# Optimization experiments

Measured on AMD Instinct MI355X. Metric: run time of the kernel, lower is better.

Reference implementation:

```python
import jax, jax.numpy as jnp
import numpy as np

B, S, D = 8, 1024, 1024  # module requires S == D for the k + w_bias broadcast
MAX_LEN = 1024


def setup_inputs() -> dict:
    key = jax.random.key(0)
    ks = jax.random.split(key, 10)
    scale = 0.02
    return {
        "x": jax.random.normal(ks[0], (B, S, D), dtype=jnp.float32),
        "wq_w": scale * jax.random.normal(ks[1], (D, D), dtype=jnp.float32),
        "wq_b": jnp.zeros((D,), dtype=jnp.float32),
        "wk_w": scale * jax.random.normal(ks[2], (D, D), dtype=jnp.float32),
        "wk_b": jnp.zeros((D,), dtype=jnp.float32),
        "wv_w": scale * jax.random.normal(ks[3], (D, D), dtype=jnp.float32),
        "wv_b": jnp.zeros((D,), dtype=jnp.float32),
        "w": 0.01 * jax.random.normal(ks[4], (MAX_LEN, MAX_LEN), dtype=jnp.float32),
        "out_w": scale * jax.random.normal(ks[5], (D, D), dtype=jnp.float32),
        "out_b": jnp.zeros((D,), dtype=jnp.float32),
    }


def reference(x, wq_w, wq_b, wk_w, wk_b, wv_w, wv_b, w, out_w, out_b):
    # torch nn.Linear: y = x @ W.T + b
    q = x @ wq_w.T + wq_b            # [B,S,D]
    k = x @ wk_w.T + wk_b            # [B,S,D]
    v = x @ wv_w.T + wv_b            # [B,S,D]
    seq_len = x.shape[1]
    w_bias = w[:seq_len, :seq_len][None]          # [1,S,S]
    # NB: original code broadcasts [B,S,D] + [1,S,S]; requires D == S.
    num = jnp.matmul(jnp.exp(k + w_bias), v)      # [B,S,D]
    den = jnp.matmul(jnp.exp(w_bias), jnp.exp(k)) # [B,S,D]
    y = jax.nn.sigmoid(q) * num / den
    return y @ out_w.T + out_b
```

## Files before the change

kernel.cpp:

```cpp
#include <hip/hip_runtime.h>
#include <hip/hip_bf16.h>


typedef float  f32x4  __attribute__((ext_vector_type(4)));
typedef short  short8 __attribute__((ext_vector_type(8)));
typedef __bf16 bf16x8 __attribute__((ext_vector_type(8)));

__device__ __forceinline__ ushort f2bf(float f){
  uint u = __builtin_bit_cast(uint, f);
  u += 0x7fffu + ((u >> 16) & 1u);
  return (ushort)(u >> 16);
}
__device__ __forceinline__ float bf2f(ushort u){
  uint v = ((uint)u) << 16;
  return __builtin_bit_cast(float, v);
}

__device__ __forceinline__ void gload16(const ushort* g, ushort* l){
  __builtin_amdgcn_global_load_lds(
      (const __attribute__((address_space(1))) void*)g,
      (__attribute__((address_space(3))) void*)l, 16, 0, 0);
}

__device__ __forceinline__ f32x4 mfma16(short8 a, short8 b, f32x4 c){
  return __builtin_amdgcn_mfma_f32_16x16x32_bf16(
      __builtin_bit_cast(bf16x8, a), __builtin_bit_cast(bf16x8, b), c, 0, 0, 0);
}

template<int EPI>
__global__ __launch_bounds__(256) void gemm_bt(
    const ushort* __restrict__ A, const ushort* __restrict__ B,
    void* __restrict__ C, const float* __restrict__ bias,
    int N, int K, long sA, long sB, long sC)
{
  __shared__ ushort As[128 * 64] __attribute__((aligned(16)));
  __shared__ ushort Bs[128 * 64] __attribute__((aligned(16)));

  const int tid  = threadIdx.x;
  const int lane = tid & 63;
  const int wid  = tid >> 6;
  const int wm   = wid >> 1;
  const int wn   = wid & 1;
  const long z   = blockIdx.z;
  const long tileM = (long)blockIdx.y * 128;
  const long tileN = (long)blockIdx.x * 128;

  const ushort* Ab = A + z * sA + tileM * K;
  const ushort* Bb = B + z * sB + tileN * K;

  long gOff[4]; int lOff[4];
#pragma unroll
  for (int j = 0; j < 4; ++j) {
    int chunk = j * 256 + tid;
    int row   = chunk >> 3;
    int c16   = (chunk & 7) ^ (row & 7);
    gOff[j]   = (long)row * K + c16 * 8;
    lOff[j]   = chunk * 8;
  }

  f32x4 acc[4][4];
#pragma unroll
  for (int i = 0; i < 4; ++i)
#pragma unroll
    for (int j = 0; j < 4; ++j) acc[i][j] = (f32x4)0.f;

  const int rA0 = wm * 64 + (lane & 15);
  const int rB0 = wn * 64 + (lane & 15);
  const int cw0 = lane >> 4;

  for (int kt = 0; kt < K; kt += 64) {
    __syncthreads();
#pragma unroll
    for (int j = 0; j < 4; ++j) {
      gload16(Ab + gOff[j] + kt, &As[lOff[j]]);
      gload16(Bb + gOff[j] + kt, &Bs[lOff[j]]);
    }
    __syncthreads();

    short8 af[4][2], bf[4][2];
#pragma unroll
    for (int f = 0; f < 4; ++f) {
      int ra = rA0 + f * 16;
      int rb = rB0 + f * 16;
#pragma unroll
      for (int kk = 0; kk < 2; ++kk) {
        af[f][kk] = *(const short8*)&As[ra * 64 + (((kk * 4 + cw0) ^ (ra & 7)) * 8)];
        bf[f][kk] = *(const short8*)&Bs[rb * 64 + (((kk * 4 + cw0) ^ (rb & 7)) * 8)];
      }
    }
#pragma unroll
    for (int kk = 0; kk < 2; ++kk)
#pragma unroll
      for (int fi = 0; fi < 4; ++fi)
#pragma unroll
        for (int fj = 0; fj < 4; ++fj)
          acc[fi][fj] = mfma16(af[fi][kk], bf[fj][kk], acc[fi][fj]);
  }

#pragma unroll
  for (int fi = 0; fi < 4; ++fi) {
    long gm0 = tileM + wm * 64 + fi * 16 + (lane >> 4) * 4;
#pragma unroll
    for (int fj = 0; fj < 4; ++fj) {
      long gn = tileN + wn * 64 + fj * 16 + (lane & 15);
      float bv = bias ? bias[gn] : 0.f;
      if (EPI == 0) {
        ushort* Cp = (ushort*)C + z * sC;
#pragma unroll
        for (int r = 0; r < 4; ++r)
          Cp[(gm0 + r) * (long)N + gn] = f2bf(acc[fi][fj][r] + bv);
      } else {
        float* Cp = (float*)C + z * sC;
#pragma unroll
        for (int r = 0; r < 4; ++r)
          Cp[(gm0 + r) * (long)N + gn] = acc[fi][fj][r] + bv;
      }
    }
  }
}

__global__ void cvt_x(const float* __restrict__ in, ushort* __restrict__ out){
  long i4 = ((long)blockIdx.x * 256 + threadIdx.x) * 4;
  float4 v = *(const float4*)&in[i4];
  ushort4 o;
  o.x = f2bf(v.x); o.y = f2bf(v.y); o.z = f2bf(v.z); o.w = f2bf(v.w);
  *(ushort4*)&out[i4] = o;
}

__global__ void prep(const float* __restrict__ wq, const float* __restrict__ wk,
                     const float* __restrict__ wv, const float* __restrict__ ow,
                     const float* __restrict__ w,
                     const float* __restrict__ bq, const float* __restrict__ bk,
                     const float* __restrict__ bv,
                     ushort* __restrict__ wcat, ushort* __restrict__ owb,
                     ushort* __restrict__ ewb, float* __restrict__ bcat)
{
  long i4 = ((long)blockIdx.x * 256 + threadIdx.x) * 4;
  const long MB = 1048576;
  if (i4 < 3 * MB) {
    const float* src = (i4 < MB) ? wq : (i4 < 2 * MB ? wk : wv);
    long off = i4 & (MB - 1);
    float4 v = *(const float4*)&src[off];
    ushort4 o; o.x=f2bf(v.x); o.y=f2bf(v.y); o.z=f2bf(v.z); o.w=f2bf(v.w);
    *(ushort4*)&wcat[i4] = o;
  } else if (i4 < 4 * MB) {
    long off = i4 - 3 * MB;
    float4 v = *(const float4*)&ow[off];
    ushort4 o; o.x=f2bf(v.x); o.y=f2bf(v.y); o.z=f2bf(v.z); o.w=f2bf(v.w);
    *(ushort4*)&owb[off] = o;
  } else if (i4 < 5 * MB) {
    long off = i4 - 4 * MB;
    float4 v = *(const float4*)&w[off];
    ushort4 o;
    o.x=f2bf(expf(v.x)); o.y=f2bf(expf(v.y)); o.z=f2bf(expf(v.z)); o.w=f2bf(expf(v.w));
    *(ushort4*)&ewb[off] = o;
  } else {
    long i = i4 - 5 * MB;
    if (i < 3072) {
      const float* src = (i < 1024) ? bq : (i < 2048 ? bk : bv);
      long off = i & 1023;
      *(float4*)&bcat[i] = *(const float4*)&src[off];
    }
  }
}

__global__ void ew_E(const ushort* __restrict__ qkv, const float* __restrict__ w,
                     ushort* __restrict__ E)
{
  long e4 = ((long)blockIdx.x * 256 + threadIdx.x) * 4;
  long m = e4 >> 10;
  int  j = (int)(e4 & 1023);
  int  s = (int)(m & 1023);
  ushort4 kv = *(const ushort4*)&qkv[m * 3072 + 1024 + j];
  float4  wv = *(const float4*)&w[(long)s * 1024 + j];
  ushort4 o;
  o.x = f2bf(expf(bf2f(kv.x) + wv.x));
  o.y = f2bf(expf(bf2f(kv.y) + wv.y));
  o.z = f2bf(expf(bf2f(kv.z) + wv.z));
  o.w = f2bf(expf(bf2f(kv.w) + wv.w));
  *(ushort4*)&E[e4] = o;
}

template<bool DOEXP>
__global__ void transpose_seg(const ushort* __restrict__ qkv,
                              ushort* __restrict__ dst, int colOff)
{
  __shared__ float tile[32][33];
  int b  = blockIdx.z;
  int s0 = blockIdx.y * 32, d0 = blockIdx.x * 32;
  int tx = threadIdx.x, ty = threadIdx.y;
#pragma unroll
  for (int i = 0; i < 4; ++i) {
    int s = s0 + ty + i * 8;
    float f = bf2f(qkv[((long)(b * 1024 + s)) * 3072 + colOff + d0 + tx]);
    if (DOEXP) f = expf(f);
    tile[ty + i * 8][tx] = f;
  }
  __syncthreads();
#pragma unroll
  for (int i = 0; i < 4; ++i) {
    int d = d0 + ty + i * 8;
    dst[((long)b * 1024 + d) * 1024 + s0 + tx] = f2bf(tile[tx][ty + i * 8]);
  }
}

__global__ void ew_y(const ushort* __restrict__ qkv, const ushort* __restrict__ num,
                     const ushort* __restrict__ den, ushort* __restrict__ y)
{
  long e4 = ((long)blockIdx.x * 256 + threadIdx.x) * 4;
  long m = e4 >> 10;
  int  d = (int)(e4 & 1023);
  ushort4 q4 = *(const ushort4*)&qkv[m * 3072 + d];
  ushort4 n4 = *(const ushort4*)&num[e4];
  ushort4 d4 = *(const ushort4*)&den[e4];
  ushort4 o;
  {
    float q = bf2f(q4.x), s = 1.f / (1.f + expf(-q));
    o.x = f2bf(s * bf2f(n4.x) / bf2f(d4.x));
  }
  {
    float q = bf2f(q4.y), s = 1.f / (1.f + expf(-q));
    o.y = f2bf(s * bf2f(n4.y) / bf2f(d4.y));
  }
  {
    float q = bf2f(q4.z), s = 1.f / (1.f + expf(-q));
    o.z = f2bf(s * bf2f(n4.z) / bf2f(d4.z));
  }
  {
    float q = bf2f(q4.w), s = 1.f / (1.f + expf(-q));
    o.w = f2bf(s * bf2f(n4.w) / bf2f(d4.w));
  }
  *(ushort4*)&y[e4] = o;
}

extern "C" void kernel_launch(void* const* d_in, const int* in_sizes, int n_in,
                              void* d_out, int out_size, void* d_ws, size_t ws_size,
                              hipStream_t stream)
{
  const float* x     = (const float*)d_in[0];
  const float* wq_w  = (const float*)d_in[1];
  const float* wq_b  = (const float*)d_in[2];
  const float* wk_w  = (const float*)d_in[3];
  const float* wk_b  = (const float*)d_in[4];
  const float* wv_w  = (const float*)d_in[5];
  const float* wv_b  = (const float*)d_in[6];
  const float* w     = (const float*)d_in[7];
  const float* out_w = (const float*)d_in[8];
  const float* out_b = (const float*)d_in[9];
  float* out = (float*)d_out;

  const long MB = 1048576;
  char* ws = (char*)d_ws;
  size_t o = 0;
  auto alloc = [&](size_t bytes){ size_t r = o; o += (bytes + 255) & ~(size_t)255; return r; };

  ushort* xb   = (ushort*)(ws + alloc(8192 * 1024 * 2));
  ushort* wcat = (ushort*)(ws + alloc(3072 * 1024 * 2));
  ushort* owb  = (ushort*)(ws + alloc(1024 * 1024 * 2));
  ushort* ewb  = (ushort*)(ws + alloc(1024 * 1024 * 2));
  float*  bcat = (float*) (ws + alloc(3072 * 4));
  ushort* qkvb = (ushort*)(ws + alloc(8192 * 3072 * 2));
  ushort* Eb   = (ushort*)(ws + alloc(8 * MB * 2));
  ushort* vTb  = (ushort*)(ws + alloc(8 * MB * 2));
  ushort* EKTb = (ushort*)(ws + alloc(8 * MB * 2));
  ushort* numb = (ushort*)(ws + alloc(8 * MB * 2));
  ushort* denb = (ushort*)(ws + alloc(8 * MB * 2));
  ushort* yb   = (ushort*)(ws + alloc(8 * MB * 2));
  (void)ws_size; (void)in_sizes; (void)n_in; (void)out_size;

  cvt_x<<<8192, 256, 0, stream>>>(x, xb);
  prep<<<5123, 256, 0, stream>>>(wq_w, wk_w, wv_w, out_w, w,
                                 wq_b, wk_b, wv_b, wcat, owb, ewb, bcat);

  gemm_bt<0><<<dim3(24, 64, 1), 256, 0, stream>>>(
      xb, wcat, qkvb, bcat, 3072, 1024, 0, 0, 0);

  ew_E<<<8192, 256, 0, stream>>>(qkvb, w, Eb);
  transpose_seg<false><<<dim3(32, 32, 8), dim3(32, 8), 0, stream>>>(qkvb, vTb, 2048);
  transpose_seg<true ><<<dim3(32, 32, 8), dim3(32, 8), 0, stream>>>(qkvb, EKTb, 1024);

  gemm_bt<0><<<dim3(8, 8, 8), 256, 0, stream>>>(
      Eb, vTb, numb, nullptr, 1024, 1024, MB, MB, MB);
  gemm_bt<0><<<dim3(8, 8, 8), 256, 0, stream>>>(
      ewb, EKTb, denb, nullptr, 1024, 1024, 0, MB, MB);

  ew_y<<<8192, 256, 0, stream>>>(qkvb, numb, denb, yb);

  gemm_bt<1><<<dim3(8, 64, 1), 256, 0, stream>>>(
      yb, owb, out, out_b, 1024, 1024, 0, 0, 0);
}
```

Before: 296.9 us.

## Add 256x256 tiled bf16 GEMM and merge num/den batched GEMMs into one launch

Introduces a 512-thread GEMM kernel with 256x256 output tiles, a 4-stage LDS ring filled by direct global-to-LDS loads, swizzled LDS layout, and split MFMA phases with priority hints. It is used for the QKV projection and for a single launch that covers both the numerator and denominator batched GEMMs through a z-split. The goal is more data reuse per tile and less launch overhead, at the cost of fewer blocks (tail and occupancy risk) and heavy register pressure from 128 accumulators per lane.

```diff
diff --git a/kernel.cpp b/kernel.cpp
--- a/kernel.cpp
+++ b/kernel.cpp
@@ -25,6 +25,126 @@
 __device__ __forceinline__ f32x4 mfma16(short8 a, short8 b, f32x4 c){
   return __builtin_amdgcn_mfma_f32_16x16x32_bf16(
       __builtin_bit_cast(bf16x8, a), __builtin_bit_cast(bf16x8, b), c, 0, 0, 0);
+}
+
+__global__ __launch_bounds__(512, 2) void gemm256(
+    const ushort* __restrict__ A0, long sA0,
+    const ushort* __restrict__ B0, long sB0,
+    ushort* __restrict__ C0, long sC0,
+    const ushort* __restrict__ A1, long sA1,
+    const ushort* __restrict__ B1, long sB1,
+    ushort* __restrict__ C1, long sC1,
+    const float* __restrict__ bias, int N, int zsplit)
+{
+  __shared__ ushort sh[65536] __attribute__((aligned(16)));
+
+  const int tid  = threadIdx.x;
+  const int lane = tid & 63;
+  const int wid  = tid >> 6;
+  const int wm   = wid >> 2;
+  const int wn   = wid & 3;
+  const long tileM = (long)blockIdx.y * 256;
+  const long tileN = (long)blockIdx.x * 256;
+  const int  z = blockIdx.z;
+
+  const ushort* Ab; const ushort* Bb; ushort* Cb;
+  if (z < zsplit) {
+    Ab = A0 + (long)z * sA0; Bb = B0 + (long)z * sB0; Cb = C0 + (long)z * sC0;
+  } else {
+    int z1 = z - zsplit;
+    Ab = A1 + (long)z1 * sA1; Bb = B1 + (long)z1 * sB1; Cb = C1 + (long)z1 * sC1;
+  }
+  Ab += tileM * 1024;
+  Bb += tileN * 1024;
+
+  long gA[2]; int lO[2];
+#pragma unroll
+  for (int j = 0; j < 2; ++j) {
+    int ch  = j * 512 + tid;
+    int row = ch >> 2, c = ch & 3;
+    int cs  = c ^ ((row >> 1) & 3);
+    gA[j] = (long)row * 1024 + cs * 8;
+    lO[j] = ch * 8;
+  }
+
+  f32x4 acc[8][4];
+#pragma unroll
+  for (int i = 0; i < 8; ++i)
+#pragma unroll
+    for (int j = 0; j < 4; ++j) acc[i][j] = (f32x4)0.f;
+
+  const int sw  = ((lane & 15) >> 1) & 3;
+  const int kq  = lane >> 4;
+  const int aoff = (wm * 128 + (lane & 15)) * 32 + ((kq ^ sw) * 8);
+  const int boff = (wn * 64  + (lane & 15)) * 32 + ((kq ^ sw) * 8);
+
+  auto stage = [&](int t) {
+    int b = (t & 3) * 8192, kt = t * 32;
+#pragma unroll
+    for (int j = 0; j < 2; ++j) {
+      gload16(Ab + gA[j] + kt, &sh[b + lO[j]]);
+      gload16(Bb + gA[j] + kt, &sh[32768 + b + lO[j]]);
+    }
+  };
+
+  stage(0); stage(1); stage(2);
+  asm volatile("s_waitcnt vmcnt(8)" ::: "memory");
+  __builtin_amdgcn_s_barrier();
+  __builtin_amdgcn_sched_barrier(0);
+
+  for (int t = 0; t < 32; ++t) {
+    if (t + 3 < 32) stage(t + 3);
+
+    const ushort* Al = &sh[(t & 3) * 8192];
+    const ushort* Bl = &sh[32768 + (t & 3) * 8192];
+
+    short8 bf[4], af0[4], af1[4];
+#pragma unroll
+    for (int j = 0; j < 4; ++j) bf[j]  = *(const short8*)&Bl[boff + j * 512];
+#pragma unroll
+    for (int j = 0; j < 4; ++j) af0[j] = *(const short8*)&Al[aoff + j * 512];
+    __builtin_amdgcn_s_barrier();
+    __builtin_amdgcn_s_setprio(1);
+#pragma unroll
+    for (int fi = 0; fi < 4; ++fi)
+#pragma unroll
+      for (int fj = 0; fj < 4; ++fj)
+        acc[fi][fj] = mfma16(af0[fi], bf[fj], acc[fi][fj]);
+    __builtin_amdgcn_s_setprio(0);
+    __builtin_amdgcn_s_barrier();
+
+#pragma unroll
+    for (int j = 0; j < 4; ++j) af1[j] = *(const short8*)&Al[aoff + (4 + j) * 512];
+    __builtin_amdgcn_s_barrier();
+    __builtin_amdgcn_s_setprio(1);
+#pragma unroll
+    for (int fi = 0; fi < 4; ++fi)
+#pragma unroll
+      for (int fj = 0; fj < 4; ++fj)
+        acc[4 + fi][fj] = mfma16(af1[fi], bf[fj], acc[4 + fi][fj]);
+    __builtin_amdgcn_s_setprio(0);
+
+    if (t < 29)       asm volatile("s_waitcnt vmcnt(8)" ::: "memory");
+    else if (t == 29) asm volatile("s_waitcnt vmcnt(4)" ::: "memory");
+    else if (t == 30) asm volatile("s_waitcnt vmcnt(0)" ::: "memory");
+    if (t < 31) {
+      __builtin_amdgcn_s_barrier();
+      __builtin_amdgcn_sched_barrier(0);
+    }
+  }
+
+#pragma unroll
+  for (int fj = 0; fj < 4; ++fj) {
+    long gn = tileN + wn * 64 + fj * 16 + (lane & 15);
+    float bv = bias ? bias[gn] : 0.f;
+#pragma unroll
+    for (int fi = 0; fi < 8; ++fi) {
+      long gm0 = tileM + wm * 128 + fi * 16 + (lane >> 4) * 4;
+#pragma unroll
+      for (int r = 0; r < 4; ++r)
+        Cb[(gm0 + r) * (long)N + gn] = f2bf(acc[fi][fj][r] + bv);
+    }
+  }
 }
 
 template<int EPI>
@@ -214,22 +334,10 @@
   ushort4 n4 = *(const ushort4*)&num[e4];
   ushort4 d4 = *(const ushort4*)&den[e4];
   ushort4 o;
-  {
-    float q = bf2f(q4.x), s = 1.f / (1.f + expf(-q));
-    o.x = f2bf(s * bf2f(n4.x) / bf2f(d4.x));
-  }
-  {
-    float q = bf2f(q4.y), s = 1.f / (1.f + expf(-q));
-    o.y = f2bf(s * bf2f(n4.y) / bf2f(d4.y));
-  }
-  {
-    float q = bf2f(q4.z), s = 1.f / (1.f + expf(-q));
-    o.z = f2bf(s * bf2f(n4.z) / bf2f(d4.z));
-  }
-  {
-    float q = bf2f(q4.w), s = 1.f / (1.f + expf(-q));
-    o.w = f2bf(s * bf2f(n4.w) / bf2f(d4.w));
-  }
+  { float q = bf2f(q4.x), s = 1.f / (1.f + expf(-q)); o.x = f2bf(s * bf2f(n4.x) / bf2f(d4.x)); }
+  { float q = bf2f(q4.y), s = 1.f / (1.f + expf(-q)); o.y = f2bf(s * bf2f(n4.y) / bf2f(d4.y)); }
+  { float q = bf2f(q4.z), s = 1.f / (1.f + expf(-q)); o.z = f2bf(s * bf2f(n4.z) / bf2f(d4.z)); }
+  { float q = bf2f(q4.w), s = 1.f / (1.f + expf(-q)); o.w = f2bf(s * bf2f(n4.w) / bf2f(d4.w)); }
   *(ushort4*)&y[e4] = o;
 }
 
@@ -272,17 +380,19 @@
   prep<<<5123, 256, 0, stream>>>(wq_w, wk_w, wv_w, out_w, w,
                                  wq_b, wk_b, wv_b, wcat, owb, ewb, bcat);
 
-  gemm_bt<0><<<dim3(24, 64, 1), 256, 0, stream>>>(
-      xb, wcat, qkvb, bcat, 3072, 1024, 0, 0, 0);
+  gemm256<<<dim3(12, 32, 1), 512, 0, stream>>>(
+      xb, 0, wcat, 0, qkvb, 0,
+      xb, 0, wcat, 0, qkvb, 0,
+      bcat, 3072, 1);
 
   ew_E<<<8192, 256, 0, stream>>>(qkvb, w, Eb);
   transpose_seg<false><<<dim3(32, 32, 8), dim3(32, 8), 0, stream>>>(qkvb, vTb, 2048);
   transpose_seg<true ><<<dim3(32, 32, 8), dim3(32, 8), 0, stream>>>(qkvb, EKTb, 1024);
 
-  gemm_bt<0><<<dim3(8, 8, 8), 256, 0, stream>>>(
-      Eb, vTb, numb, nullptr, 1024, 1024, MB, MB, MB);
-  gemm_bt<0><<<dim3(8, 8, 8), 256, 0, stream>>>(
-      ewb, EKTb, denb, nullptr, 1024, 1024, 0, MB, MB);
+  gemm256<<<dim3(4, 4, 16), 512, 0, stream>>>(
+      Eb,  MB, vTb,  MB, numb, MB,
+      ewb, 0,  EKTb, MB, denb, MB,
+      nullptr, 1024, 8);
 
   ew_y<<<8192, 256, 0, stream>>>(qkvb, numb, denb, yb);
 
```

After: 307.4 us. 3.5% more time.

## Fuse elementwise kernels, merge num/den GEMMs, add XCD-aware block remapping

Applied to the files above, without the earlier changes.

Merges the x-conversion and weight-prep kernels into one launch, and fuses the exp(k+w) elementwise kernel with both transposes (v and exp(k)) into a single pass over qkv. Batches the numerator and denominator GEMMs into one grid-split launch. Adds an XCD-aware workgroup remapping in the GEMM so neighbouring tiles land on the same XCD for L2 reuse. The goals are lower launch overhead, fewer redundant reads of qkv, and better cache locality. The cost is more index arithmetic, and E is now written with scalar rather than vectorised stores.

```diff
diff --git a/kernel.cpp b/kernel.cpp
--- a/kernel.cpp
+++ b/kernel.cpp
@@ -29,24 +29,47 @@
 
 template<int EPI>
 __global__ __launch_bounds__(256) void gemm_bt(
-    const ushort* __restrict__ A, const ushort* __restrict__ B,
-    void* __restrict__ C, const float* __restrict__ bias,
-    int N, int K, long sA, long sB, long sC)
+    const ushort* __restrict__ A0, long sA0,
+    const ushort* __restrict__ B0, long sB0,
+    void* __restrict__ C0, long sC0, const float* __restrict__ bias0,
+    const ushort* __restrict__ A1, long sA1,
+    const ushort* __restrict__ B1, long sB1,
+    void* __restrict__ C1, long sC1, const float* __restrict__ bias1,
+    int N, int K, int zsplit)
 {
   __shared__ ushort As[128 * 64] __attribute__((aligned(16)));
   __shared__ ushort Bs[128 * 64] __attribute__((aligned(16)));
+
+  const int nx = gridDim.x, ny = gridDim.y;
+  const long nwg = (long)nx * ny * gridDim.z;
+  const long lid = ((long)blockIdx.z * ny + blockIdx.y) * nx + blockIdx.x;
+  const long q8 = nwg >> 3, r8 = nwg & 7;
+  const long xcd = lid & 7, idx = lid >> 3;
+  const long sid = (xcd < r8 ? xcd * (q8 + 1) : r8 * (q8 + 1) + (xcd - r8) * q8) + idx;
+  const int bx = (int)(sid % nx);
+  const long t1 = sid / nx;
+  const int by = (int)(t1 % ny);
+  const int bz = (int)(t1 / ny);
 
   const int tid  = threadIdx.x;
   const int lane = tid & 63;
   const int wid  = tid >> 6;
   const int wm   = wid >> 1;
   const int wn   = wid & 1;
-  const long z   = blockIdx.z;
-  const long tileM = (long)blockIdx.y * 128;
-  const long tileN = (long)blockIdx.x * 128;
-
-  const ushort* Ab = A + z * sA + tileM * K;
-  const ushort* Bb = B + z * sB + tileN * K;
+  const long tileM = (long)by * 128;
+  const long tileN = (long)bx * 128;
+
+  const ushort* Ab; const ushort* Bb; void* Cb; const float* bias;
+  if (bz < zsplit) {
+    Ab = A0 + (long)bz * sA0; Bb = B0 + (long)bz * sB0;
+    Cb = (char*)C0 + (long)bz * sC0 * (EPI ? 4 : 2); bias = bias0;
+  } else {
+    long z1 = bz - zsplit;
+    Ab = A1 + z1 * sA1; Bb = B1 + z1 * sB1;
+    Cb = (char*)C1 + z1 * sC1 * (EPI ? 4 : 2); bias = bias1;
+  }
+  Ab += tileM * K;
+  Bb += tileN * K;
 
   long gOff[4]; int lOff[4];
 #pragma unroll
@@ -105,12 +128,12 @@
       long gn = tileN + wn * 64 + fj * 16 + (lane & 15);
       float bv = bias ? bias[gn] : 0.f;
       if (EPI == 0) {
-        ushort* Cp = (ushort*)C + z * sC;
+        ushort* Cp = (ushort*)Cb;
 #pragma unroll
         for (int r = 0; r < 4; ++r)
           Cp[(gm0 + r) * (long)N + gn] = f2bf(acc[fi][fj][r] + bv);
       } else {
-        float* Cp = (float*)C + z * sC;
+        float* Cp = (float*)Cb;
 #pragma unroll
         for (int r = 0; r < 4; ++r)
           Cp[(gm0 + r) * (long)N + gn] = acc[fi][fj][r] + bv;
@@ -119,43 +142,44 @@
   }
 }
 
-__global__ void cvt_x(const float* __restrict__ in, ushort* __restrict__ out){
+__global__ void prep_all(const float* __restrict__ x,
+                         const float* __restrict__ wq, const float* __restrict__ wk,
+                         const float* __restrict__ wv, const float* __restrict__ ow,
+                         const float* __restrict__ w,
+                         const float* __restrict__ bq, const float* __restrict__ bk,
+                         const float* __restrict__ bv,
+                         ushort* __restrict__ xb,
+                         ushort* __restrict__ wcat, ushort* __restrict__ owb,
+                         ushort* __restrict__ ewb, float* __restrict__ bcat)
+{
+  const long MB = 1048576;
   long i4 = ((long)blockIdx.x * 256 + threadIdx.x) * 4;
-  float4 v = *(const float4*)&in[i4];
-  ushort4 o;
-  o.x = f2bf(v.x); o.y = f2bf(v.y); o.z = f2bf(v.z); o.w = f2bf(v.w);
-  *(ushort4*)&out[i4] = o;
-}
-
-__global__ void prep(const float* __restrict__ wq, const float* __restrict__ wk,
-                     const float* __restrict__ wv, const float* __restrict__ ow,
-                     const float* __restrict__ w,
-                     const float* __restrict__ bq, const float* __restrict__ bk,
-                     const float* __restrict__ bv,
-                     ushort* __restrict__ wcat, ushort* __restrict__ owb,
-                     ushort* __restrict__ ewb, float* __restrict__ bcat)
-{
-  long i4 = ((long)blockIdx.x * 256 + threadIdx.x) * 4;
-  const long MB = 1048576;
-  if (i4 < 3 * MB) {
-    const float* src = (i4 < MB) ? wq : (i4 < 2 * MB ? wk : wv);
-    long off = i4 & (MB - 1);
+  if (i4 < 8 * MB) {
+    float4 v = *(const float4*)&x[i4];
+    ushort4 o; o.x=f2bf(v.x); o.y=f2bf(v.y); o.z=f2bf(v.z); o.w=f2bf(v.w);
+    *(ushort4*)&xb[i4] = o;
+    return;
+  }
+  long j4 = i4 - 8 * MB;
+  if (j4 < 3 * MB) {
+    const float* src = (j4 < MB) ? wq : (j4 < 2 * MB ? wk : wv);
+    long off = j4 & (MB - 1);
     float4 v = *(const float4*)&src[off];
     ushort4 o; o.x=f2bf(v.x); o.y=f2bf(v.y); o.z=f2bf(v.z); o.w=f2bf(v.w);
-    *(ushort4*)&wcat[i4] = o;
-  } else if (i4 < 4 * MB) {
-    long off = i4 - 3 * MB;
+    *(ushort4*)&wcat[j4] = o;
+  } else if (j4 < 4 * MB) {
+    long off = j4 - 3 * MB;
     float4 v = *(const float4*)&ow[off];
     ushort4 o; o.x=f2bf(v.x); o.y=f2bf(v.y); o.z=f2bf(v.z); o.w=f2bf(v.w);
     *(ushort4*)&owb[off] = o;
-  } else if (i4 < 5 * MB) {
-    long off = i4 - 4 * MB;
+  } else if (j4 < 5 * MB) {
+    long off = j4 - 4 * MB;
     float4 v = *(const float4*)&w[off];
     ushort4 o;
     o.x=f2bf(expf(v.x)); o.y=f2bf(expf(v.y)); o.z=f2bf(expf(v.z)); o.w=f2bf(expf(v.w));
     *(ushort4*)&ewb[off] = o;
   } else {
-    long i = i4 - 5 * MB;
+    long i = j4 - 5 * MB;
     if (i < 3072) {
       const float* src = (i < 1024) ? bq : (i < 2048 ? bk : bv);
       long off = i & 1023;
@@ -164,43 +188,33 @@
   }
 }
 
-__global__ void ew_E(const ushort* __restrict__ qkv, const float* __restrict__ w,
-                     ushort* __restrict__ E)
-{
-  long e4 = ((long)blockIdx.x * 256 + threadIdx.x) * 4;
-  long m = e4 >> 10;
-  int  j = (int)(e4 & 1023);
-  int  s = (int)(m & 1023);
-  ushort4 kv = *(const ushort4*)&qkv[m * 3072 + 1024 + j];
-  float4  wv = *(const float4*)&w[(long)s * 1024 + j];
-  ushort4 o;
-  o.x = f2bf(expf(bf2f(kv.x) + wv.x));
-  o.y = f2bf(expf(bf2f(kv.y) + wv.y));
-  o.z = f2bf(expf(bf2f(kv.z) + wv.z));
-  o.w = f2bf(expf(bf2f(kv.w) + wv.w));
-  *(ushort4*)&E[e4] = o;
-}
-
-template<bool DOEXP>
-__global__ void transpose_seg(const ushort* __restrict__ qkv,
-                              ushort* __restrict__ dst, int colOff)
-{
-  __shared__ float tile[32][33];
+__global__ void mid(const ushort* __restrict__ qkv, const float* __restrict__ w,
+                    ushort* __restrict__ E, ushort* __restrict__ vT,
+                    ushort* __restrict__ EKT)
+{
+  __shared__ float tk[32][33];
+  __shared__ float tv[32][33];
   int b  = blockIdx.z;
   int s0 = blockIdx.y * 32, d0 = blockIdx.x * 32;
   int tx = threadIdx.x, ty = threadIdx.y;
 #pragma unroll
   for (int i = 0; i < 4; ++i) {
     int s = s0 + ty + i * 8;
-    float f = bf2f(qkv[((long)(b * 1024 + s)) * 3072 + colOff + d0 + tx]);
-    if (DOEXP) f = expf(f);
-    tile[ty + i * 8][tx] = f;
+    long base = ((long)(b * 1024 + s)) * 3072;
+    float kf = bf2f(qkv[base + 1024 + d0 + tx]);
+    float vf = bf2f(qkv[base + 2048 + d0 + tx]);
+    tk[ty + i * 8][tx] = expf(kf);
+    tv[ty + i * 8][tx] = vf;
+    float wv = w[(long)s * 1024 + d0 + tx];
+    E[((long)(b * 1024 + s)) * 1024 + d0 + tx] = f2bf(expf(kf + wv));
   }
   __syncthreads();
 #pragma unroll
   for (int i = 0; i < 4; ++i) {
     int d = d0 + ty + i * 8;
-    dst[((long)b * 1024 + d) * 1024 + s0 + tx] = f2bf(tile[tx][ty + i * 8]);
+    long o = ((long)b * 1024 + d) * 1024 + s0 + tx;
+    EKT[o] = f2bf(tk[tx][ty + i * 8]);
+    vT [o] = f2bf(tv[tx][ty + i * 8]);
   }
 }
 
@@ -214,22 +228,10 @@
   ushort4 n4 = *(const ushort4*)&num[e4];
   ushort4 d4 = *(const ushort4*)&den[e4];
   ushort4 o;
-  {
-    float q = bf2f(q4.x), s = 1.f / (1.f + expf(-q));
-    o.x = f2bf(s * bf2f(n4.x) / bf2f(d4.x));
-  }
-  {
-    float q = bf2f(q4.y), s = 1.f / (1.f + expf(-q));
-    o.y = f2bf(s * bf2f(n4.y) / bf2f(d4.y));
-  }
-  {
-    float q = bf2f(q4.z), s = 1.f / (1.f + expf(-q));
-    o.z = f2bf(s * bf2f(n4.z) / bf2f(d4.z));
-  }
-  {
-    float q = bf2f(q4.w), s = 1.f / (1.f + expf(-q));
-    o.w = f2bf(s * bf2f(n4.w) / bf2f(d4.w));
-  }
+  { float qv = bf2f(q4.x), s = 1.f / (1.f + expf(-qv)); o.x = f2bf(s * bf2f(n4.x) / bf2f(d4.x)); }
+  { float qv = bf2f(q4.y), s = 1.f / (1.f + expf(-qv)); o.y = f2bf(s * bf2f(n4.y) / bf2f(d4.y)); }
+  { float qv = bf2f(q4.z), s = 1.f / (1.f + expf(-qv)); o.z = f2bf(s * bf2f(n4.z) / bf2f(d4.z)); }
+  { float qv = bf2f(q4.w), s = 1.f / (1.f + expf(-qv)); o.w = f2bf(s * bf2f(n4.w) / bf2f(d4.w)); }
   *(ushort4*)&y[e4] = o;
 }
 
@@ -268,24 +270,26 @@
   ushort* yb   = (ushort*)(ws + alloc(8 * MB * 2));
   (void)ws_size; (void)in_sizes; (void)n_in; (void)out_size;
 
-  cvt_x<<<8192, 256, 0, stream>>>(x, xb);
-  prep<<<5123, 256, 0, stream>>>(wq_w, wk_w, wv_w, out_w, w,
-                                 wq_b, wk_b, wv_b, wcat, owb, ewb, bcat);
+  prep_all<<<13315, 256, 0, stream>>>(x, wq_w, wk_w, wv_w, out_w, w,
+                                      wq_b, wk_b, wv_b,
+                                      xb, wcat, owb, ewb, bcat);
 
   gemm_bt<0><<<dim3(24, 64, 1), 256, 0, stream>>>(
-      xb, wcat, qkvb, bcat, 3072, 1024, 0, 0, 0);
-
-  ew_E<<<8192, 256, 0, stream>>>(qkvb, w, Eb);
-  transpose_seg<false><<<dim3(32, 32, 8), dim3(32, 8), 0, stream>>>(qkvb, vTb, 2048);
-  transpose_seg<true ><<<dim3(32, 32, 8), dim3(32, 8), 0, stream>>>(qkvb, EKTb, 1024);
-
-  gemm_bt<0><<<dim3(8, 8, 8), 256, 0, stream>>>(
-      Eb, vTb, numb, nullptr, 1024, 1024, MB, MB, MB);
-  gemm_bt<0><<<dim3(8, 8, 8), 256, 0, stream>>>(
-      ewb, EKTb, denb, nullptr, 1024, 1024, 0, MB, MB);
+      xb, 0, wcat, 0, qkvb, 0, bcat,
+      xb, 0, wcat, 0, qkvb, 0, bcat,
+      3072, 1024, 1);
+
+  mid<<<dim3(32, 32, 8), dim3(32, 8), 0, stream>>>(qkvb, w, Eb, vTb, EKTb);
+
+  gemm_bt<0><<<dim3(8, 8, 16), 256, 0, stream>>>(
+      Eb,  MB, vTb,  MB, numb, MB, nullptr,
+      ewb, 0,  EKTb, MB, denb, MB, nullptr,
+      1024, 1024, 8);
 
   ew_y<<<8192, 256, 0, stream>>>(qkvb, numb, denb, yb);
 
   gemm_bt<1><<<dim3(8, 64, 1), 256, 0, stream>>>(
-      yb, owb, out, out_b, 1024, 1024, 0, 0, 0);
-}
+      yb, 0, owb, 0, out, 0, out_b,
+      yb, 0, owb, 0, out, 0, out_b,
+      1024, 1024, 1);
+}
```

Measured after the change: 288.1 us. 1.03x faster.
